# Kernel optimization log

Hardware: AMD Instinct MI355X
Metric: run time of the kernel (lower is better)

The kernel has to match this reference:

```python
import jax, jax.numpy as jnp
import numpy as np
from itertools import product

EPS = 1e-6
P = 3  # heatmap_size; corr channels = P**3 = 27


def l2_on_axis(x, axis=1):
    return jnp.sqrt(jnp.sum(x * x, axis=axis, keepdims=True) + EPS)


def reduce_masked_mean(x, mask):
    return jnp.sum(x * mask) / (jnp.sum(mask) + EPS)


def smoothl1(d):
    a = jnp.abs(d)
    return jnp.where(a < 1.0, 0.5 * d * d, a - 0.5)


def corr3d(f0, f1):
    # 3D correlation volume, patch P^3, zero padding. (B,C,D,H,W)->(B,P^3,D,H,W)
    B, C, D, H, W = f0.shape
    pad = P // 2
    f1p = jnp.pad(f1, ((0, 0), (0, 0), (pad, pad), (pad, pad), (pad, pad)))
    outs = []
    for dz in range(P):
        for dy in range(P):
            for dx in range(P):
                s = f1p[:, :, dz:dz + D, dy:dy + H, dx:dx + W]
                outs.append(jnp.einsum('bcdhw,bcdhw->bdhw', f0, s))
    return jnp.stack(outs, axis=1)


def flow_head(cc, W1, b1, W2, b2):
    cc = jax.nn.relu(cc)
    cc = cc / (jnp.sqrt(jnp.sum(cc * cc, axis=1, keepdims=True)) + EPS)  # l2_normalize dim=1
    h = jnp.einsum('oc,bcdhw->bodhw', W1, cc) + b1[None, :, None, None, None]
    h = jnp.where(h > 0, h, 0.01 * h)  # LeakyReLU
    return jnp.einsum('oc,bcdhw->bodhw', W2, h) + b2[None, :, None, None, None]


def backwarp(feat, flow):
    # trilinear backwarp, zero padding outside; flow ch: (dx->W, dy->H, dz->D)
    B, C, D, H, W = feat.shape
    zz, yy, xx = jnp.meshgrid(jnp.arange(D, dtype=flow.dtype),
                              jnp.arange(H, dtype=flow.dtype),
                              jnp.arange(W, dtype=flow.dtype), indexing='ij')
    xs = xx[None] + flow[:, 0]
    ys = yy[None] + flow[:, 1]
    zs = zz[None] + flow[:, 2]
    x0, y0, z0 = jnp.floor(xs), jnp.floor(ys), jnp.floor(zs)
    featf = feat.reshape(B, C, D * H * W)
    out = jnp.zeros_like(feat)
    for cz, cy, cx in product((0, 1), (0, 1), (0, 1)):
        zi, yi, xi = z0 + cz, y0 + cy, x0 + cx
        w = (1 - jnp.abs(zs - zi)) * (1 - jnp.abs(ys - yi)) * (1 - jnp.abs(xs - xi))
        valid = ((zi >= 0) & (zi < D) & (yi >= 0) & (yi < H) & (xi >= 0) & (xi < W)).astype(feat.dtype)
        idx = ((jnp.clip(zi, 0, D - 1) * H + jnp.clip(yi, 0, H - 1)) * W
               + jnp.clip(xi, 0, W - 1)).astype(jnp.int32).reshape(B, -1)
        g = jnp.take_along_axis(featf, idx[:, None, :], axis=2).reshape(B, C, D, H, W)
        out = out + g * (w * valid)[:, None]
    return out


def gradient3d_abs(x):
    dz = jnp.abs(jnp.pad(x[:, :, 1:] - x[:, :, :-1], ((0, 0), (0, 0), (0, 1), (0, 0), (0, 0))))
    dy = jnp.abs(jnp.pad(x[:, :, :, 1:] - x[:, :, :, :-1], ((0, 0), (0, 0), (0, 0), (0, 1), (0, 0))))
    dx = jnp.abs(jnp.pad(x[:, :, :, :, 1:] - x[:, :, :, :, :-1], ((0, 0), (0, 0), (0, 0), (0, 0), (0, 1))))
    return dx, dy, dz


def setup_inputs() -> dict:
    key = jax.random.key(0)
    ks = jax.random.split(key, 8)
    B, C, D, H, W = 2, 32, 64, 64, 64
    return {
        'feat0': jax.random.normal(ks[0], (B, C, D, H, W), jnp.float32),
        'feat1': jax.random.normal(ks[1], (B, C, D, H, W), jnp.float32),
        'flow_g': jax.random.normal(ks[2], (B, 3, D, H, W), jnp.float32),
        'mask_g': jax.random.uniform(ks[3], (B, 1, D, H, W), jnp.float32),
        'W1': jax.random.normal(ks[4], (64, P ** 3), jnp.float32) * 0.05,
        'b1': jnp.zeros((64,), jnp.float32),
        'W2': jax.random.normal(ks[5], (3, 64), jnp.float32) * 0.05,
        'b2': jnp.zeros((3,), jnp.float32),
        'is_synth': 0,
    }


def reference(feat0, feat1, flow_g, mask_g, W1, b1, W2, b2, is_synth):
    B, C, D, H, W = feat0.shape
    # hinge loss (feat1_aligned == feat1 at iteration 0)
    hinge_vox = jax.nn.relu(0.2 - l2_on_axis(feat1 - feat0))
    hinge_mask = (jnp.sum(jnp.abs(flow_g), axis=1, keepdims=True) > 1.0).astype(feat0.dtype)
    hinge_loss = reduce_masked_mean(hinge_vox, hinge_mask)

    # single scale sc=1.0
    flow_forw = flow_head(corr3d(feat0, feat1), W1, b1, W2, b2)
    flow_back = flow_head(corr3d(feat1, feat0), W1, b1, W2, b2)

    feat1_aligned = backwarp(feat1, flow_forw)
    ones1 = jnp.ones((B, 1, D, H, W), feat0.dtype)
    valid1 = backwarp(ones1, flow_forw)
    valid0 = backwarp(ones1, flow_forw)  # faithful: source also uses flow_total_forw

    feat_diff = reduce_masked_mean(l2_on_axis(feat1_aligned - feat0), valid1 * valid0)
    warp_loss_cumu = feat_diff  # * sc (=1)

    l1_diff = jnp.mean(smoothl1(flow_forw - flow_g), axis=1, keepdims=True)
    l2_diff = jnp.mean((flow_forw - flow_g) ** 2, axis=1, keepdims=True)
    nonzero = (jnp.sum(jnp.abs(flow_g), axis=1, keepdims=True) > 0.01).astype(feat0.dtype) * mask_g
    yeszero = (1.0 - nonzero) * mask_g
    l1_bal = 0.5 * (reduce_masked_mean(l1_diff, nonzero) + reduce_masked_mean(l1_diff, yeszero))
    l2_bal = 0.5 * (reduce_masked_mean(l2_diff, nonzero) + reduce_masked_mean(l2_diff, yeszero))

    fb_al = backwarp(flow_back, jax.lax.stop_gradient(flow_forw))
    ff_al = backwarp(flow_forw, jax.lax.stop_gradient(flow_back))
    cycle_loss = jnp.mean(smoothl1(flow_forw + fb_al)) + jnp.mean(smoothl1(flow_back + ff_al))

    dx, dy, dz = gradient3d_abs(flow_forw)
    smooth_forw = jnp.mean(dx + dy + dx, axis=1, keepdims=True)  # faithful: dx counted twice
    dx, dy, dz = gradient3d_abs(flow_back)
    smooth_back = jnp.mean(dx + dy + dx, axis=1, keepdims=True)
    smooth_loss = jnp.mean((smooth_forw + smooth_back) * 0.5)

    # all hyp coefficients = 1.0; is_synth selects identical coeffs here
    total_loss = hinge_loss + cycle_loss + l1_bal + l2_bal + warp_loss_cumu + smooth_loss
    return total_loss, flow_forw
```

## Files before the change

kernel.cpp:

```cpp
#include <hip/hip_runtime.h>
#include <math.h>

#define EPSF 1e-6f

typedef __attribute__((ext_vector_type(8))) short short8;
typedef __attribute__((ext_vector_type(4))) float f32x4;

constexpr int Bn = 2, Cn = 32, Dn = 64, Hn = 64, Wn = 64;
constexpr int HW  = Hn * Wn;
constexpr int DHW = Dn * HW;
constexpr int NVOX = Bn * DHW;


__device__ inline float sl1(float d) {
    float a = fabsf(d);
    return a < 1.f ? 0.5f * d * d : a - 0.5f;
}

__device__ inline float dpp_left(float v) {
    int r = __builtin_amdgcn_update_dpp(0, __float_as_int(v), 0x138 ,
                                        0xF, 0xF, true);
    return __int_as_float(r);
}
__device__ inline float dpp_right(float v) {
    int r = __builtin_amdgcn_update_dpp(0, __float_as_int(v), 0x130 ,
                                        0xF, 0xF, true);
    return __int_as_float(r);
}

__device__ inline unsigned int bf16b(float f) {
    return (__float_as_uint(f) + 0x8000u) >> 16;
}
__device__ inline unsigned int bfpack(float lo, float hi) {
    return bf16b(lo) | ((__float_as_uint(hi) + 0x8000u) & 0xffff0000u);
}
__device__ inline float bf2f(unsigned short u) {
    return __uint_as_float((unsigned int)u << 16);
}

struct PairGather {
    int   pidx[4];
    int   sel[4];
    float w0[4], w1[4];
};

__device__ inline void warp_pair_setup(float flx, float fly, float flz,
                                       int x, int y, int z,
                                       PairGather& pg, float& wsum) {
    float xs = (float)x + flx, ys = (float)y + fly, zs = (float)z + flz;
    float xf = floorf(xs), yf = floorf(ys), zf = floorf(zs);
    float fx = xs - xf, fy = ys - yf, fz = zs - zf;
    int xi = (int)xf, yi = (int)yf, zi = (int)zf;

    int x0c = min(max(xi, 0), Wn - 1);
    bool xv0 = (xi >= 0) && (xi < Wn);
    bool xv1 = (xi + 1 >= 0) && (xi + 1 < Wn);
    int sel = (xi >= 0 && xi < Wn - 1) ? 1 : 0;
    float wx0 = xv0 ? (1.f - fx) : 0.f;
    float wx1 = xv1 ? fx : 0.f;

    wsum = 0.f;
#pragma unroll
    for (int cz = 0; cz < 2; cz++) {
        int zz = zi + cz;
        bool zv = (zz >= 0) && (zz < Dn);
        int zc = min(max(zz, 0), Dn - 1);
        float wz = (cz ? fz : 1.f - fz) * (zv ? 1.f : 0.f);
#pragma unroll
        for (int cy = 0; cy < 2; cy++) {
            int yy = yi + cy;
            bool yv = (yy >= 0) && (yy < Hn);
            int yc = min(max(yy, 0), Hn - 1);
            float wy = (cy ? fy : 1.f - fy) * (yv ? 1.f : 0.f);
            int k = cz * 2 + cy;
            int sp = (zc * Hn + yc) * Wn + x0c;
            pg.pidx[k] = min(sp, DHW - 2);
            pg.sel[k] = sel;
            float wzy = wz * wy;
            pg.w0[k] = wzy * wx0;
            pg.w1[k] = wzy * wx1;
            wsum += pg.w0[k] + pg.w1[k];
        }
    }
}

__device__ inline float gather8(const float* __restrict__ slab, const PairGather& pg) {
    float g = 0.f;
#pragma unroll
    for (int k = 0; k < 4; k++) {
        float2 v = *reinterpret_cast<const float2*>(slab + pg.pidx[k]);
        float second = pg.sel[k] ? v.y : v.x;
        g = fmaf(v.x, pg.w0[k], g);
        g = fmaf(second, pg.w1[k], g);
    }
    return g;
}

__global__ void prep_kernel(const float* __restrict__ W1, ushort* __restrict__ W1bf) {
    int i = blockIdx.x * 256 + threadIdx.x;
    if (i < 64 * 32) {
        int n = i >> 5, k = i & 31;
        float val = (k < 27) ? W1[n * 27 + k] : 0.f;
        W1bf[n * 40 + k] = (ushort)bf16b(val);
    }
}

__device__ __forceinline__ void flow_head_mfma(
        float* acc, ushort (&ccS)[4][64][40], int wid, int lane,
        const ushort* __restrict__ W1bf, const float* __restrict__ b1,
        const float* __restrict__ W2, const float* __restrict__ b2,
        float* __restrict__ flow_out, size_t fb0,
        float& mfx, float& mfy, float& mfz) {
    float ss = 0.f;
#pragma unroll
    for (int i = 0; i < 27; i++) {
        float r = acc[i] > 0.f ? acc[i] : 0.f;
        acc[i] = r;
        ss = fmaf(r, r, ss);
    }
    float inv = 1.0f / (sqrtf(ss) + EPSF);
#pragma unroll
    for (int i = 0; i < 27; i++) acc[i] *= inv;

    {
        unsigned int pk[16];
#pragma unroll
        for (int i = 0; i < 13; i++) pk[i] = bfpack(acc[2 * i], acc[2 * i + 1]);
        pk[13] = bfpack(acc[26], 0.f);
        pk[14] = 0u; pk[15] = 0u;
        uint2* rowp = reinterpret_cast<uint2*>(&ccS[wid][lane][0]);
#pragma unroll
        for (int i = 0; i < 8; i++) rowp[i] = make_uint2(pk[2 * i], pk[2 * i + 1]);
    }

    int c0 = lane & 15, oct = lane >> 4;

    short8 bfr[4];
#pragma unroll
    for (int t = 0; t < 4; t++)
        bfr[t] = *reinterpret_cast<const short8*>(W1bf + (size_t)(t * 16 + c0) * 40 + oct * 8);

    f32x4 b1v[4], w2f0[4], w2f1[4], w2f2[4];
#pragma unroll
    for (int mt = 0; mt < 4; mt++) {
        b1v[mt]  = *reinterpret_cast<const f32x4*>(b1 + mt * 16 + oct * 4);
        w2f0[mt] = *reinterpret_cast<const f32x4*>(W2 + mt * 16 + oct * 4);
        w2f1[mt] = *reinterpret_cast<const f32x4*>(W2 + 64 + mt * 16 + oct * 4);
        w2f2[mt] = *reinterpret_cast<const f32x4*>(W2 + 128 + mt * 16 + oct * 4);
    }
    float bb0 = b2[0], bb1 = b2[1], bb2 = b2[2];

#pragma unroll
    for (int nt = 0; nt < 4; nt++) {
        short8 afr = *reinterpret_cast<const short8*>(&ccS[wid][nt * 16 + c0][oct * 8]);
        f32x4 ac[4];
#pragma unroll
        for (int mt = 0; mt < 4; mt++) {
            f32x4 zero = {0.f, 0.f, 0.f, 0.f};
            ac[mt] = __builtin_amdgcn_mfma_f32_16x16x32_bf16(bfr[mt], afr, zero, 0, 0, 0);
        }
        float p0 = 0.f, p1 = 0.f, p2 = 0.f;
#pragma unroll
        for (int mt = 0; mt < 4; mt++) {
#pragma unroll
            for (int rg = 0; rg < 4; rg++) {
                float h = ac[mt][rg] + b1v[mt][rg];
                h = fmaxf(h, 0.01f * h);
                p0 = fmaf(w2f0[mt][rg], h, p0);
                p1 = fmaf(w2f1[mt][rg], h, p1);
                p2 = fmaf(w2f2[mt][rg], h, p2);
            }
        }
        p0 += __shfl_xor(p0, 16); p0 += __shfl_xor(p0, 32);
        p1 += __shfl_xor(p1, 16); p1 += __shfl_xor(p1, 32);
        p2 += __shfl_xor(p2, 16); p2 += __shfl_xor(p2, 32);
        if (oct == nt) {
            int vox = nt * 16 + c0;
            mfx = p0 + bb0; mfy = p1 + bb1; mfz = p2 + bb2;
            flow_out[fb0 + vox]           = mfx;
            flow_out[fb0 + DHW + vox]     = mfy;
            flow_out[fb0 + 2 * DHW + vox] = mfz;
        }
    }
}

__global__ __launch_bounds__(256)
void corr_fwd_kernel(const float* __restrict__ feat0, const float* __restrict__ feat1,
                     const ushort* __restrict__ W1bf, const float* __restrict__ b1,
                     const float* __restrict__ W2, const float* __restrict__ b2,
                     float* __restrict__ flow_forw,
                     const float* __restrict__ flow_g, const float* __restrict__ mask_g,
                     float* __restrict__ accum, ushort* __restrict__ craw) {
    __shared__ ushort ccS[4][64][40];

    int tid = threadIdx.x;
    int lane = tid & 63;
    int wid = __builtin_amdgcn_readfirstlane(tid >> 6);

    int R = blockIdx.x * 4 + wid;
    int y = R & 63, z = (R >> 6) & 63, b = R >> 12;

    const float* rp[9];
    float rmask[9];
    {
        int idx = 0;
#pragma unroll
        for (int dz = -1; dz <= 1; dz++) {
#pragma unroll
            for (int dy = -1; dy <= 1; dy++, idx++) {
                int zz = z + dz, yy = y + dy;
                bool valid = (zz >= 0) && (zz < Dn) && (yy >= 0) && (yy < Hn);
                int zc = min(max(zz, 0), Dn - 1);
                int yc = min(max(yy, 0), Hn - 1);
                rp[idx] = feat1 + (size_t)b * Cn * DHW + (size_t)zc * HW + (size_t)yc * Wn;
                rmask[idx] = valid ? 1.f : 0.f;
            }
        }
    }
    const float* ap = feat0 + (size_t)b * Cn * DHW + (size_t)z * HW + (size_t)y * Wn;

    float C[9], TL[9], TR[9];
#pragma unroll
    for (int r = 0; r < 9; r++) { C[r] = 0.f; TL[r] = 0.f; TR[r] = 0.f; }
    float diff2 = 0.f;

#pragma unroll 2
    for (int c = 0; c < Cn; c++) {
        float a = ap[lane];
        float rowv[9];
#pragma unroll
        for (int r = 0; r < 9; r++) rowv[r] = rp[r][lane];
        ap += DHW;
#pragma unroll
        for (int r = 0; r < 9; r++) rp[r] += DHW;

        float aL = dpp_left(a);
        float aR = dpp_right(a);
        float d = rowv[4] - a;
        diff2 = fmaf(d, d, diff2);
#pragma unroll
        for (int r = 0; r < 9; r++) {
            float rv = rowv[r];
            C[r]  = fmaf(a,  rv, C[r]);
            TL[r] = fmaf(aL, rv, TL[r]);
            TR[r] = fmaf(aR, rv, TR[r]);
        }
    }

    float acc[27];
#pragma unroll
    for (int r = 0; r < 9; r++) {
        acc[r * 3 + 0] = dpp_left(TR[r]) * rmask[r];
        acc[r * 3 + 1] = C[r] * rmask[r];
        acc[r * 3 + 2] = dpp_right(TL[r]) * rmask[r];
    }

    size_t vidx = (size_t)R * 64 + lane;
#pragma unroll
    for (int i = 0; i < 27; i++)
        craw[(size_t)i * NVOX + vidx] = (ushort)bf16b(acc[i]);

    size_t fb0 = (size_t)b * 3 * DHW + (size_t)z * HW + (size_t)y * Wn;
    float mfx, mfy, mfz;
    flow_head_mfma(acc, ccS, wid, lane, W1bf, b1, W2, b2, flow_forw, fb0,
                   mfx, mfy, mfz);

    size_t fbase = fb0 + lane;
    float gx = flow_g[fbase], gy = flow_g[fbase + DHW], gz = flow_g[fbase + 2 * DHW];
    float mg = mask_g[(size_t)b * DHW + (size_t)z * HW + y * Wn + lane];

    float ag = fabsf(gx) + fabsf(gy) + fabsf(gz);
    float hmask = ag > 1.0f ? 1.f : 0.f;
    float hv = 0.2f - sqrtf(diff2 + EPSF);
    hv = hv > 0.f ? hv : 0.f;

    float dx0 = mfx - gx, dy0 = mfy - gy, dz0 = mfz - gz;
    float l1 = (sl1(dx0) + sl1(dy0) + sl1(dz0)) * (1.f / 3.f);
    float l2 = (dx0 * dx0 + dy0 * dy0 + dz0 * dz0) * (1.f / 3.f);
    float nz = (ag > 0.01f ? 1.f : 0.f) * mg;
    float yz = (1.f - nz) * mg;

    PairGather pgF; float wsum;
    warp_pair_setup(mfx, mfy, mfz, lane, y, z, pgF, wsum);
    const float* f1b = feat0 ;
    f1b = feat1 + (size_t)b * Cn * DHW;
    const float* f0c = feat0 + (size_t)b * Cn * DHW + (size_t)z * HW + y * Wn + lane;
    float s = 0.f;
#pragma unroll 4
    for (int c = 0; c < Cn; c++) {
        float g = gather8(f1b + (size_t)c * DHW, pgF);
        float d = g - f0c[(size_t)c * DHW];
        s = fmaf(d, d, s);
    }
    float vm = wsum * wsum;
    float wnum = sqrtf(s + EPSF) * vm;

    float pv[10];
    pv[0] = hv * hmask; pv[1] = hmask;
    pv[2] = wnum;       pv[3] = vm;
    pv[4] = l1 * nz;    pv[5] = l1 * yz;
    pv[6] = l2 * nz;    pv[7] = l2 * yz;
    pv[8] = nz;         pv[9] = yz;

#pragma unroll
    for (int i = 0; i < 10; i++) {
        float val = pv[i];
        for (int off = 32; off; off >>= 1) val += __shfl_down(val, off, 64);
        pv[i] = val;
    }
    __shared__ float sred[10][4];
    if (lane == 0) {
#pragma unroll
        for (int i = 0; i < 10; i++) sred[i][wid] = pv[i];
    }
    __syncthreads();
    if (tid < 10) {
        atomicAdd(&accum[tid], sred[tid][0] + sred[tid][1] + sred[tid][2] + sred[tid][3]);
    }
}

__global__ __launch_bounds__(256)
void corr_bwd_kernel(const ushort* __restrict__ craw,
                     const ushort* __restrict__ W1bf, const float* __restrict__ b1,
                     const float* __restrict__ W2, const float* __restrict__ b2,
                     float* __restrict__ flow_back) {
    __shared__ ushort ccS[4][64][40];

    int tid = threadIdx.x;
    int lane = tid & 63;
    int wid = __builtin_amdgcn_readfirstlane(tid >> 6);

    int R = blockIdx.x * 4 + wid;
    int y = R & 63, z = (R >> 6) & 63, b = R >> 12;

    float acc[27];
#pragma unroll
    for (int sz = 0; sz < 3; sz++) {
#pragma unroll
        for (int sy = 0; sy < 3; sy++) {
            int zz = z + sz - 1, yy = y + sy - 1;
            bool valid = (zz >= 0) && (zz < Dn) && (yy >= 0) && (yy < Hn);
            int zc = min(max(zz, 0), Dn - 1);
            int yc = min(max(yy, 0), Hn - 1);
            float m = valid ? 1.f : 0.f;
            const ushort* rowb = craw + (size_t)b * DHW + (size_t)zc * HW + (size_t)yc * Wn + lane;
            int base = (sz * 3 + sy) * 3;
            float v0 = bf2f(rowb[(size_t)(26 - base) * NVOX]);
            float v1 = bf2f(rowb[(size_t)(25 - base) * NVOX]);
            float v2 = bf2f(rowb[(size_t)(24 - base) * NVOX]);
            acc[base + 0] = dpp_left(v0) * m;
            acc[base + 1] = v1 * m;
            acc[base + 2] = dpp_right(v2) * m;
        }
    }

    size_t fb0 = (size_t)b * 3 * DHW + (size_t)z * HW + (size_t)y * Wn;
    float mfx, mfy, mfz;
    flow_head_mfma(acc, ccS, wid, lane, W1bf, b1, W2, b2, flow_back, fb0,
                   mfx, mfy, mfz);
}

__global__ __launch_bounds__(256)
void slim_loss_kernel(const float* __restrict__ flowf, const float* __restrict__ flowb,
                      float* __restrict__ accum) {
    int tid = threadIdx.x;
    int v = blockIdx.x * 256 + tid;
    int x = v & 63, y = (v >> 6) & 63, z = (v >> 12) & 63, b = v >> 18;

    size_t sp = (size_t)z * HW + y * Wn + x;
    size_t f3 = (size_t)b * 3 * DHW + sp;

    float ffx = flowf[f3], ffy = flowf[f3 + DHW], ffz = flowf[f3 + 2 * DHW];
    float fbx = flowb[f3], fby = flowb[f3 + DHW], fbz = flowb[f3 + 2 * DHW];

    PairGather pgF; float wsumF;
    warp_pair_setup(ffx, ffy, ffz, x, y, z, pgF, wsumF);
    const float* fb_b = flowb + (size_t)b * 3 * DHW;
    float fbalx = gather8(fb_b, pgF);
    float fbaly = gather8(fb_b + DHW, pgF);
    float fbalz = gather8(fb_b + 2 * DHW, pgF);
    float cyc1 = sl1(ffx + fbalx) + sl1(ffy + fbaly) + sl1(ffz + fbalz);

    PairGather pgB; float wsumB;
    warp_pair_setup(fbx, fby, fbz, x, y, z, pgB, wsumB);
    const float* ff_b = flowf + (size_t)b * 3 * DHW;
    float ffalx = gather8(ff_b, pgB);
    float ffaly = gather8(ff_b + DHW, pgB);
    float ffalz = gather8(ff_b + 2 * DHW, pgB);
    float cyc2 = sl1(fbx + ffalx) + sl1(fby + ffaly) + sl1(fbz + ffalz);

    float sf = 0.f, sb2v = 0.f;
#pragma unroll
    for (int j = 0; j < 3; j++) {
        const float* pf = flowf + f3 + (size_t)j * DHW;
        float c0 = pf[0];
        float ddx = (x < Wn - 1) ? fabsf(pf[1] - c0) : 0.f;
        float ddy = (y < Hn - 1) ? fabsf(pf[Wn] - c0) : 0.f;
        sf += 2.f * ddx + ddy;
        const float* pb = flowb + f3 + (size_t)j * DHW;
        float c1 = pb[0];
        float ddx2 = (x < Wn - 1) ? fabsf(pb[1] - c1) : 0.f;
        float ddy2 = (y < Hn - 1) ? fabsf(pb[Wn] - c1) : 0.f;
        sb2v += 2.f * ddx2 + ddy2;
    }
    float smoothv = 0.5f * (sf * (1.f / 3.f) + sb2v * (1.f / 3.f));

    float pv[3] = { cyc1, cyc2, smoothv };
#pragma unroll
    for (int i = 0; i < 3; i++) {
        float val = pv[i];
        for (int off = 32; off; off >>= 1) val += __shfl_down(val, off, 64);
        pv[i] = val;
    }
    __shared__ float sred[3][4];
    int lane = tid & 63, wid = tid >> 6;
    if (lane == 0) {
#pragma unroll
        for (int i = 0; i < 3; i++) sred[i][wid] = pv[i];
    }
    __syncthreads();
    if (tid < 3) {
        atomicAdd(&accum[10 + tid], sred[tid][0] + sred[tid][1] + sred[tid][2] + sred[tid][3]);
    }
}

__global__ void finalize_kernel(const float* __restrict__ accum, float* __restrict__ out) {
    float hinge = accum[0] / (accum[1] + EPSF);
    float warp  = accum[2] / (accum[3] + EPSF);
    float l1b = 0.5f * (accum[4] / (accum[8] + EPSF) + accum[5] / (accum[9] + EPSF));
    float l2b = 0.5f * (accum[6] / (accum[8] + EPSF) + accum[7] / (accum[9] + EPSF));
    float n3 = 3.0f * (float)NVOX;
    float cyc = accum[10] / n3 + accum[11] / n3;
    float sm  = accum[12] / (float)NVOX;
    out[0] = hinge + cyc + l1b + l2b + warp + sm;
}

extern "C" void kernel_launch(void* const* d_in, const int* in_sizes, int n_in,
                              void* d_out, int out_size, void* d_ws, size_t ws_size,
                              hipStream_t stream) {
    const float* feat0  = (const float*)d_in[0];
    const float* feat1  = (const float*)d_in[1];
    const float* flow_g = (const float*)d_in[2];
    const float* mask_g = (const float*)d_in[3];
    const float* W1     = (const float*)d_in[4];
    const float* b1     = (const float*)d_in[5];
    const float* W2     = (const float*)d_in[6];
    const float* b2     = (const float*)d_in[7];

    float* out = (float*)d_out;
    float* accum = (float*)d_ws;
    ushort* W1bf = (ushort*)((char*)d_ws + 128);
    const size_t FLOWB_OFF = 8192;
    const size_t FLOWB_BYTES = (size_t)Bn * 3 * DHW * sizeof(float);
    float* flow_back = (float*)((char*)d_ws + FLOWB_OFF);
    const size_t CRAW_OFF = FLOWB_OFF + FLOWB_BYTES;
    const size_t CRAW_BYTES = (size_t)27 * NVOX * sizeof(ushort);
    ushort* craw = (ushort*)((char*)d_ws + CRAW_OFF);
    float* flow_forw = out + 1;

    hipMemsetAsync(d_ws, 0, 64, stream);

    dim3 block(256);
    prep_kernel<<<dim3(8), block, 0, stream>>>(W1, W1bf);

    corr_fwd_kernel<<<dim3(NVOX / 256), block, 0, stream>>>(
        feat0, feat1, W1bf, b1, W2, b2, flow_forw, flow_g, mask_g, accum, craw);
    corr_bwd_kernel<<<dim3(NVOX / 256), block, 0, stream>>>(
        craw, W1bf, b1, W2, b2, flow_back);
    slim_loss_kernel<<<dim3(NVOX / 256), block, 0, stream>>>(flow_forw, flow_back, accum);
    finalize_kernel<<<1, 1, 0, stream>>>(accum, out);
}
```

Baseline: 163.9 us.

## Pack feat1 into bf16 channel-interleaved layout and swizzle blocks across XCDs

Adds a pack kernel that converts feat1 to bf16 with four channels interleaved per 8-byte word. The correlation and warp-gather loops then read this packed buffer instead of fp32 planes, which halves feat1 traffic and cuts the number of load instructions. Block indices in all main kernels are also remapped so that neighbouring rows land on the same XCD, which should improve L2 reuse. The packing pass is extra work, and using bf16 for feat1 lowers the precision of the correlation and warp loss.

```diff
diff --git a/kernel.cpp b/kernel.cpp
--- a/kernel.cpp
+++ b/kernel.cpp
@@ -10,6 +10,7 @@
 constexpr int HW  = Hn * Wn;
 constexpr int DHW = Dn * HW;
 constexpr int NVOX = Bn * DHW;
+constexpr size_t BS = (size_t)Cn * DHW;
 
 
 __device__ inline float sl1(float d) {
@@ -17,14 +18,16 @@
     return a < 1.f ? 0.5f * d * d : a - 0.5f;
 }
 
+__device__ inline int xcd_swz(int bid, int chunk) {
+    return (bid & 7) * chunk + (bid >> 3);
+}
+
 __device__ inline float dpp_left(float v) {
-    int r = __builtin_amdgcn_update_dpp(0, __float_as_int(v), 0x138 ,
-                                        0xF, 0xF, true);
+    int r = __builtin_amdgcn_update_dpp(0, __float_as_int(v), 0x138, 0xF, 0xF, true);
     return __int_as_float(r);
 }
 __device__ inline float dpp_right(float v) {
-    int r = __builtin_amdgcn_update_dpp(0, __float_as_int(v), 0x130 ,
-                                        0xF, 0xF, true);
+    int r = __builtin_amdgcn_update_dpp(0, __float_as_int(v), 0x130, 0xF, 0xF, true);
     return __int_as_float(r);
 }
 
@@ -36,6 +39,11 @@
 }
 __device__ inline float bf2f(unsigned short u) {
     return __uint_as_float((unsigned int)u << 16);
+}
+__device__ inline float unpk(uint2 q, int j) {
+    unsigned w = (j < 2) ? q.x : q.y;
+    return (j & 1) ? __uint_as_float(w & 0xffff0000u)
+                   : __uint_as_float(w << 16);
 }
 
 struct PairGather {
@@ -105,8 +113,24 @@
     }
 }
 
+__global__ __launch_bounds__(256)
+void pack_kernel(const float* __restrict__ f1, uint2* __restrict__ pk1) {
+    int v = blockIdx.x * 256 + threadIdx.x;
+    int b = v >> 18;
+    int sp = v & (DHW - 1);
+    const float* src = f1 + (size_t)b * BS + sp;
+#pragma unroll
+    for (int p = 0; p < 8; p++) {
+        float c0 = src[(size_t)(4 * p + 0) * DHW];
+        float c1 = src[(size_t)(4 * p + 1) * DHW];
+        float c2 = src[(size_t)(4 * p + 2) * DHW];
+        float c3 = src[(size_t)(4 * p + 3) * DHW];
+        pk1[(size_t)p * NVOX + v] = make_uint2(bfpack(c0, c1), bfpack(c2, c3));
+    }
+}
+
 __device__ __forceinline__ void flow_head_mfma(
-        float* acc, ushort (&ccS)[4][64][40], int wid, int lane,
+        float* acc, ushort (*ccS)[64][40], int wid, int lane,
         const ushort* __restrict__ W1bf, const float* __restrict__ b1,
         const float* __restrict__ W2, const float* __restrict__ b2,
         float* __restrict__ flow_out, size_t fb0,
@@ -184,8 +208,33 @@
     }
 }
 
+__device__ __forceinline__ void fwd_losses_common(
+        float mfx, float mfy, float mfz, float diff2,
+        const float* __restrict__ flow_g, const float* __restrict__ mask_g,
+        int lane, int y, int z, int b, size_t fb0, float* pv) {
+    size_t fbase = fb0 + lane;
+    float gx = flow_g[fbase], gy = flow_g[fbase + DHW], gz = flow_g[fbase + 2 * DHW];
+    float mg = mask_g[(size_t)b * DHW + (size_t)z * HW + y * Wn + lane];
+
+    float ag = fabsf(gx) + fabsf(gy) + fabsf(gz);
+    float hmask = ag > 1.0f ? 1.f : 0.f;
+    float hv = 0.2f - sqrtf(diff2 + EPSF);
+    hv = hv > 0.f ? hv : 0.f;
+
+    float dx0 = mfx - gx, dy0 = mfy - gy, dz0 = mfz - gz;
+    float l1 = (sl1(dx0) + sl1(dy0) + sl1(dz0)) * (1.f / 3.f);
+    float l2 = (dx0 * dx0 + dy0 * dy0 + dz0 * dz0) * (1.f / 3.f);
+    float nz = (ag > 0.01f ? 1.f : 0.f) * mg;
+    float yz = (1.f - nz) * mg;
+
+    pv[0] = hv * hmask; pv[1] = hmask;
+    pv[4] = l1 * nz;    pv[5] = l1 * yz;
+    pv[6] = l2 * nz;    pv[7] = l2 * yz;
+    pv[8] = nz;         pv[9] = yz;
+}
+
 __global__ __launch_bounds__(256)
-void corr_fwd_kernel(const float* __restrict__ feat0, const float* __restrict__ feat1,
+void corr_fwd_packed(const float* __restrict__ feat0, const uint2* __restrict__ pk1,
                      const ushort* __restrict__ W1bf, const float* __restrict__ b1,
                      const float* __restrict__ W2, const float* __restrict__ b2,
                      float* __restrict__ flow_forw,
@@ -197,10 +246,10 @@
     int lane = tid & 63;
     int wid = __builtin_amdgcn_readfirstlane(tid >> 6);
 
-    int R = blockIdx.x * 4 + wid;
+    int R = xcd_swz(blockIdx.x, 256) * 4 + wid;
     int y = R & 63, z = (R >> 6) & 63, b = R >> 12;
 
-    const float* rp[9];
+    const uint2* rp[9];
     float rmask[9];
     {
         int idx = 0;
@@ -212,12 +261,152 @@
                 bool valid = (zz >= 0) && (zz < Dn) && (yy >= 0) && (yy < Hn);
                 int zc = min(max(zz, 0), Dn - 1);
                 int yc = min(max(yy, 0), Hn - 1);
-                rp[idx] = feat1 + (size_t)b * Cn * DHW + (size_t)zc * HW + (size_t)yc * Wn;
+                rp[idx] = pk1 + (size_t)b * DHW + (size_t)zc * HW + (size_t)yc * Wn;
                 rmask[idx] = valid ? 1.f : 0.f;
             }
         }
     }
-    const float* ap = feat0 + (size_t)b * Cn * DHW + (size_t)z * HW + (size_t)y * Wn;
+    const float* ap = feat0 + (size_t)b * BS + (size_t)z * HW + (size_t)y * Wn;
+
+    float C[9], TL[9], TR[9];
+#pragma unroll
+    for (int r = 0; r < 9; r++) { C[r] = 0.f; TL[r] = 0.f; TR[r] = 0.f; }
+    float diff2 = 0.f;
+
+#pragma unroll 1
+    for (int p = 0; p < 8; p++) {
+        uint2 q[9];
+#pragma unroll
+        for (int r = 0; r < 9; r++) q[r] = rp[r][lane];
+        float a4[4];
+#pragma unroll
+        for (int j = 0; j < 4; j++) a4[j] = ap[(size_t)j * DHW + lane];
+        ap += (size_t)4 * DHW;
+#pragma unroll
+        for (int r = 0; r < 9; r++) rp[r] += NVOX;
+
+#pragma unroll
+        for (int j = 0; j < 4; j++) {
+            float a = a4[j];
+            float aL = dpp_left(a), aR = dpp_right(a);
+            float ctr = unpk(q[4], j);
+            float d = ctr - a;
+            diff2 = fmaf(d, d, diff2);
+#pragma unroll
+            for (int r = 0; r < 9; r++) {
+                float rv = unpk(q[r], j);
+                C[r]  = fmaf(a,  rv, C[r]);
+                TL[r] = fmaf(aL, rv, TL[r]);
+                TR[r] = fmaf(aR, rv, TR[r]);
+            }
+        }
+    }
+
+    float acc[27];
+#pragma unroll
+    for (int r = 0; r < 9; r++) {
+        acc[r * 3 + 0] = dpp_left(TR[r]) * rmask[r];
+        acc[r * 3 + 1] = C[r] * rmask[r];
+        acc[r * 3 + 2] = dpp_right(TL[r]) * rmask[r];
+    }
+
+    size_t vidx = (size_t)R * 64 + lane;
+#pragma unroll
+    for (int i = 0; i < 27; i++)
+        craw[(size_t)i * NVOX + vidx] = (ushort)bf16b(acc[i]);
+
+    size_t fb0 = (size_t)b * 3 * DHW + (size_t)z * HW + (size_t)y * Wn;
+    float mfx, mfy, mfz;
+    flow_head_mfma(acc, ccS, wid, lane, W1bf, b1, W2, b2, flow_forw, fb0,
+                   mfx, mfy, mfz);
+
+    float pv[10];
+    fwd_losses_common(mfx, mfy, mfz, diff2, flow_g, mask_g, lane, y, z, b, fb0, pv);
+
+    {
+        PairGather pgF; float wsum;
+        warp_pair_setup(mfx, mfy, mfz, lane, y, z, pgF, wsum);
+        const uint2* slab0 = pk1 + (size_t)b * DHW;
+        const float* f0c = feat0 + (size_t)b * BS + (size_t)z * HW + (size_t)y * Wn + lane;
+        float s = 0.f;
+#pragma unroll 1
+        for (int p = 0; p < 8; p++) {
+            const uint2* slab = slab0 + (size_t)p * NVOX;
+            float g4[4] = {0.f, 0.f, 0.f, 0.f};
+#pragma unroll
+            for (int k = 0; k < 4; k++) {
+                uint2 q0 = slab[pgF.pidx[k]];
+                uint2 q1 = slab[pgF.pidx[k] + 1];
+#pragma unroll
+                for (int j = 0; j < 4; j++) {
+                    float v0 = unpk(q0, j);
+                    float v1 = pgF.sel[k] ? unpk(q1, j) : v0;
+                    g4[j] = fmaf(v0, pgF.w0[k], g4[j]);
+                    g4[j] = fmaf(v1, pgF.w1[k], g4[j]);
+                }
+            }
+#pragma unroll
+            for (int j = 0; j < 4; j++) {
+                float d = g4[j] - f0c[(size_t)(4 * p + j) * DHW];
+                s = fmaf(d, d, s);
+            }
+        }
+        float vm = wsum * wsum;
+        pv[2] = sqrtf(s + EPSF) * vm;
+        pv[3] = vm;
+    }
+
+#pragma unroll
+    for (int i = 0; i < 10; i++) {
+        float val = pv[i];
+        for (int off = 32; off; off >>= 1) val += __shfl_down(val, off, 64);
+        pv[i] = val;
+    }
+    __shared__ float sred[10][4];
+    if (lane == 0) {
+#pragma unroll
+        for (int i = 0; i < 10; i++) sred[i][wid] = pv[i];
+    }
+    __syncthreads();
+    if (tid < 10) {
+        atomicAdd(&accum[tid], sred[tid][0] + sred[tid][1] + sred[tid][2] + sred[tid][3]);
+    }
+}
+
+__global__ __launch_bounds__(256)
+void corr_fwd_f32(const float* __restrict__ feat0, const float* __restrict__ feat1,
+                  const ushort* __restrict__ W1bf, const float* __restrict__ b1,
+                  const float* __restrict__ W2, const float* __restrict__ b2,
+                  float* __restrict__ flow_forw,
+                  const float* __restrict__ flow_g, const float* __restrict__ mask_g,
+                  float* __restrict__ accum, ushort* __restrict__ craw) {
+    __shared__ ushort ccS[4][64][40];
+
+    int tid = threadIdx.x;
+    int lane = tid & 63;
+    int wid = __builtin_amdgcn_readfirstlane(tid >> 6);
+
+    int R = xcd_swz(blockIdx.x, 256) * 4 + wid;
+    int y = R & 63, z = (R >> 6) & 63, b = R >> 12;
+
+    const float* rp[9];
+    float rmask[9];
+    {
+        int idx = 0;
+#pragma unroll
+        for (int dz = -1; dz <= 1; dz++) {
+#pragma unroll
+            for (int dy = -1; dy <= 1; dy++, idx++) {
+                int zz = z + dz, yy = y + dy;
+                bool valid = (zz >= 0) && (zz < Dn) && (yy >= 0) && (yy < Hn);
+                int zc = min(max(zz, 0), Dn - 1);
+                int yc = min(max(yy, 0), Hn - 1);
+                rp[idx] = feat1 + (size_t)b * BS + (size_t)zc * HW + (size_t)yc * Wn;
+                rmask[idx] = valid ? 1.f : 0.f;
+            }
+        }
+    }
+    const float* ap = feat0 + (size_t)b * BS + (size_t)z * HW + (size_t)y * Wn;
 
     float C[9], TL[9], TR[9];
 #pragma unroll
@@ -234,8 +423,7 @@
 #pragma unroll
         for (int r = 0; r < 9; r++) rp[r] += DHW;
 
-        float aL = dpp_left(a);
-        float aR = dpp_right(a);
+        float aL = dpp_left(a), aR = dpp_right(a);
         float d = rowv[4] - a;
         diff2 = fmaf(d, d, diff2);
 #pragma unroll
@@ -265,42 +453,25 @@
     flow_head_mfma(acc, ccS, wid, lane, W1bf, b1, W2, b2, flow_forw, fb0,
                    mfx, mfy, mfz);
 
-    size_t fbase = fb0 + lane;
-    float gx = flow_g[fbase], gy = flow_g[fbase + DHW], gz = flow_g[fbase + 2 * DHW];
-    float mg = mask_g[(size_t)b * DHW + (size_t)z * HW + y * Wn + lane];
-
-    float ag = fabsf(gx) + fabsf(gy) + fabsf(gz);
-    float hmask = ag > 1.0f ? 1.f : 0.f;
-    float hv = 0.2f - sqrtf(diff2 + EPSF);
-    hv = hv > 0.f ? hv : 0.f;
-
-    float dx0 = mfx - gx, dy0 = mfy - gy, dz0 = mfz - gz;
-    float l1 = (sl1(dx0) + sl1(dy0) + sl1(dz0)) * (1.f / 3.f);
-    float l2 = (dx0 * dx0 + dy0 * dy0 + dz0 * dz0) * (1.f / 3.f);
-    float nz = (ag > 0.01f ? 1.f : 0.f) * mg;
-    float yz = (1.f - nz) * mg;
-
-    PairGather pgF; float wsum;
-    warp_pair_setup(mfx, mfy, mfz, lane, y, z, pgF, wsum);
-    const float* f1b = feat0 ;
-    f1b = feat1 + (size_t)b * Cn * DHW;
-    const float* f0c = feat0 + (size_t)b * Cn * DHW + (size_t)z * HW + y * Wn + lane;
-    float s = 0.f;
+    float pv[10];
+    fwd_losses_common(mfx, mfy, mfz, diff2, flow_g, mask_g, lane, y, z, b, fb0, pv);
+
+    {
+        PairGather pgF; float wsum;
+        warp_pair_setup(mfx, mfy, mfz, lane, y, z, pgF, wsum);
+        const float* f1b = feat1 + (size_t)b * BS;
+        const float* f0c = feat0 + (size_t)b * BS + (size_t)z * HW + (size_t)y * Wn + lane;
+        float s = 0.f;
 #pragma unroll 4
-    for (int c = 0; c < Cn; c++) {
-        float g = gather8(f1b + (size_t)c * DHW, pgF);
-        float d = g - f0c[(size_t)c * DHW];
-        s = fmaf(d, d, s);
-    }
-    float vm = wsum * wsum;
-    float wnum = sqrtf(s + EPSF) * vm;
-
-    float pv[10];
-    pv[0] = hv * hmask; pv[1] = hmask;
-    pv[2] = wnum;       pv[3] = vm;
-    pv[4] = l1 * nz;    pv[5] = l1 * yz;
-    pv[6] = l2 * nz;    pv[7] = l2 * yz;
-    pv[8] = nz;         pv[9] = yz;
+        for (int c = 0; c < Cn; c++) {
+            float g = gather8(f1b + (size_t)c * DHW, pgF);
+            float d = g - f0c[(size_t)c * DHW];
+            s = fmaf(d, d, s);
+        }
+        float vm = wsum * wsum;
+        pv[2] = sqrtf(s + EPSF) * vm;
+        pv[3] = vm;
+    }
 
 #pragma unroll
     for (int i = 0; i < 10; i++) {
@@ -324,13 +495,13 @@
                      const ushort* __restrict__ W1bf, const float* __restrict__ b1,
                      const float* __restrict__ W2, const float* __restrict__ b2,
                      float* __restrict__ flow_back) {
-    __shared__ ushort ccS[4][64][40];
+    __shared__ ushort ccSb[4][64][40];
 
     int tid = threadIdx.x;
     int lane = tid & 63;
     int wid = __builtin_amdgcn_readfirstlane(tid >> 6);
 
-    int R = blockIdx.x * 4 + wid;
+    int R = xcd_swz(blockIdx.x, 256) * 4 + wid;
     int y = R & 63, z = (R >> 6) & 63, b = R >> 12;
 
     float acc[27];
@@ -356,7 +527,7 @@
 
     size_t fb0 = (size_t)b * 3 * DHW + (size_t)z * HW + (size_t)y * Wn;
     float mfx, mfy, mfz;
-    flow_head_mfma(acc, ccS, wid, lane, W1bf, b1, W2, b2, flow_back, fb0,
+    flow_head_mfma(acc, ccSb, wid, lane, W1bf, b1, W2, b2, flow_back, fb0,
                    mfx, mfy, mfz);
 }
 
@@ -364,7 +535,7 @@
 void slim_loss_kernel(const float* __restrict__ flowf, const float* __restrict__ flowb,
                       float* __restrict__ accum) {
     int tid = threadIdx.x;
-    int v = blockIdx.x * 256 + tid;
+    int v = xcd_swz(blockIdx.x, 256) * 256 + tid;
     int x = v & 63, y = (v >> 6) & 63, z = (v >> 12) & 63, b = v >> 18;
 
     size_t sp = (size_t)z * HW + y * Wn + x;
@@ -456,17 +627,25 @@
     const size_t CRAW_OFF = FLOWB_OFF + FLOWB_BYTES;
     const size_t CRAW_BYTES = (size_t)27 * NVOX * sizeof(ushort);
     ushort* craw = (ushort*)((char*)d_ws + CRAW_OFF);
+    const size_t PK1_OFF = CRAW_OFF + CRAW_BYTES;
+    const size_t PK1_BYTES = (size_t)Cn * NVOX * sizeof(ushort);
+    uint2* pk1 = (uint2*)((char*)d_ws + PK1_OFF);
     float* flow_forw = out + 1;
 
     hipMemsetAsync(d_ws, 0, 64, stream);
 
-    dim3 block(256);
-    prep_kernel<<<dim3(8), block, 0, stream>>>(W1, W1bf);
-
-    corr_fwd_kernel<<<dim3(NVOX / 256), block, 0, stream>>>(
-        feat0, feat1, W1bf, b1, W2, b2, flow_forw, flow_g, mask_g, accum, craw);
-    corr_bwd_kernel<<<dim3(NVOX / 256), block, 0, stream>>>(
+    prep_kernel<<<dim3(8), dim3(256), 0, stream>>>(W1, W1bf);
+
+    if (ws_size >= PK1_OFF + PK1_BYTES) {
+        pack_kernel<<<dim3(NVOX / 256), dim3(256), 0, stream>>>(feat1, pk1);
+        corr_fwd_packed<<<dim3(NVOX / 256), dim3(256), 0, stream>>>(
+            feat0, pk1, W1bf, b1, W2, b2, flow_forw, flow_g, mask_g, accum, craw);
+    } else {
+        corr_fwd_f32<<<dim3(NVOX / 256), dim3(256), 0, stream>>>(
+            feat0, feat1, W1bf, b1, W2, b2, flow_forw, flow_g, mask_g, accum, craw);
+    }
+    corr_bwd_kernel<<<dim3(NVOX / 256), dim3(256), 0, stream>>>(
         craw, W1bf, b1, W2, b2, flow_back);
-    slim_loss_kernel<<<dim3(NVOX / 256), block, 0, stream>>>(flow_forw, flow_back, accum);
+    slim_loss_kernel<<<dim3(NVOX / 256), dim3(256), 0, stream>>>(flow_forw, flow_back, accum);
     finalize_kernel<<<1, 1, 0, stream>>>(accum, out);
 }
```

Result: faster. 139.9 us, median of 2 (-14.7%).
